# Kernel tuning notes

Hardware: AMD Instinct MI355X
Metric: run time of the kernel (lower is better)

## Reference

```python
import jax, jax.numpy as jnp
import numpy as np

TAU = 1.0
ATOL = 1e-06
MAX_ITER = 64  # bisection halves the bracket each iter; 64 iters reaches fp32 precision
N_WORKERS = 64
D = 2097152  # 2**21 coordinates


def setup_inputs() -> dict:
    key = jax.random.key(0)
    y = jax.random.normal(key, (N_WORKERS, D), dtype=jnp.float32)
    return {"y": y}


def reference(y) -> jnp.ndarray:
    # Coordinate-wise smooth (erf-based) median via bisection.
    # torch code transposes y and reduces over the last dim; equivalently we
    # reduce over the worker axis (axis 0) and keep per-coordinate state [d].
    xl = jnp.min(y, axis=0)  # [d] lower bracket
    xg = jnp.max(y, axis=0)  # [d] upper bracket

    def body(_, carry):
        xl, xg = carry
        xm = 0.5 * (xl + xg)                                  # [d]
        fm = jnp.sum(jax.lax.erf((y - xm) / TAU), axis=0)     # [d]
        left = fm > 0
        xl = jnp.where(left, xm, xl)
        xg = jnp.where(left, xg, xm)
        return xl, xg

    # Fixed trip count (no host-sync early exit). After MAX_ITER=64 halvings the
    # bracket width is far below the torch atol=1e-6 break threshold, so the
    # result matches the torch early-exit version to well within atol.
    xl, xg = jax.lax.fori_loop(0, MAX_ITER, body, (xl, xg))
    return 0.5 * (xl + xg)  # [d]
```

## Files before the change

### kernel.cpp

```cpp
#include <hip/hip_runtime.h>

typedef float v2f __attribute__((ext_vector_type(2)));

#define NW 64
#define NP 32
#define MAX_EVALS 8
#define FREEZE_TOL 7e-3f

__global__ __launch_bounds__(256, 4) void damed_median_kernel(
    const float* __restrict__ y, float* __restrict__ out, int D) {
  int d = blockIdx.x * blockDim.x + threadIdx.x;
  if (d >= D) return;

  v2f v[NP];
  v2f vmin = {3.4e38f, 3.4e38f}, vmax = {-3.4e38f, -3.4e38f}, sum2 = {0.f, 0.f};
#pragma unroll
  for (int p = 0; p < NP; ++p) {
    v2f t;
    t.x = y[(size_t)(2 * p) * (size_t)D + (size_t)d];
    t.y = y[(size_t)(2 * p + 1) * (size_t)D + (size_t)d];
    v[p] = t;
    vmin = __builtin_elementwise_min(vmin, t);
    vmax = __builtin_elementwise_max(vmax, t);
    sum2 += t;
  }
  float xl = fminf(vmin.x, vmin.y);
  float xg = fmaxf(vmax.x, vmax.y);
  float x = (sum2.x + sum2.y) * (1.0f / NW);
  x = fminf(fmaxf(x, xl), xg);

  const float B1 = 0.278393f, B2 = 0.230389f, B3 = 0.000972f, B4 = 0.078108f;
  const v2f one2 = {1.f, 1.f};
  const v2f Q1 = {B1, B1}, Q2 = {B2, B2}, Q3 = {B3, B3}, Q4 = {B4, B4};
  const v2f P1 = {B1, B1}, P2 = {2 * B2, 2 * B2};
  const v2f P3 = {3 * B3, 3 * B3}, P4 = {4 * B4, 4 * B4};

  auto evalF = [&](float xc) -> float {
    v2f fmA = {0.f, 0.f}, fmB = {0.f, 0.f};
    v2f nx = {-xc, -xc};
#pragma unroll
    for (int p = 0; p < NP; p += 2) {
      v2f tA = v[p] + nx;
      v2f tB = v[p + 1] + nx;
      v2f aA = __builtin_elementwise_max(tA, -tA);
      v2f aB = __builtin_elementwise_max(tB, -tB);
      v2f qA = __builtin_elementwise_fma(aA, Q4, Q3);
      v2f qB = __builtin_elementwise_fma(aB, Q4, Q3);
      qA = __builtin_elementwise_fma(aA, qA, Q2);
      qB = __builtin_elementwise_fma(aB, qB, Q2);
      qA = __builtin_elementwise_fma(aA, qA, Q1);
      qB = __builtin_elementwise_fma(aB, qB, Q1);
      qA = __builtin_elementwise_fma(aA, qA, one2);
      qB = __builtin_elementwise_fma(aB, qB, one2);
      v2f m = qA * qB;
      v2f r;
      r.x = __builtin_amdgcn_rcpf(m.x); r.y = __builtin_amdgcn_rcpf(m.y);
      v2f rA = r * qB;
      v2f rB = r * qA;
      rA = rA * rA; rB = rB * rB;
      rA = rA * rA; rB = rB * rB;
      v2f eA = one2 - rA;
      v2f eB = one2 - rB;
      eA.x = __builtin_copysignf(eA.x, tA.x); eA.y = __builtin_copysignf(eA.y, tA.y);
      eB.x = __builtin_copysignf(eB.x, tB.x); eB.y = __builtin_copysignf(eB.y, tB.y);
      fmA += eA; fmB += eB;
    }
    v2f s = fmA + fmB;
    return s.x + s.y;
  };

  float fm0, fd0;
  {
    v2f fmA = {0.f, 0.f}, fmB = {0.f, 0.f}, fdA = {0.f, 0.f}, fdB = {0.f, 0.f};
    v2f nx = {-x, -x};
#pragma unroll
    for (int p = 0; p < NP; p += 2) {
      v2f tA = v[p] + nx;
      v2f tB = v[p + 1] + nx;
      v2f aA = __builtin_elementwise_max(tA, -tA);
      v2f aB = __builtin_elementwise_max(tB, -tB);
      v2f qA = __builtin_elementwise_fma(aA, Q4, Q3);
      v2f qB = __builtin_elementwise_fma(aB, Q4, Q3);
      qA = __builtin_elementwise_fma(aA, qA, Q2);
      qB = __builtin_elementwise_fma(aB, qB, Q2);
      qA = __builtin_elementwise_fma(aA, qA, Q1);
      qB = __builtin_elementwise_fma(aB, qB, Q1);
      qA = __builtin_elementwise_fma(aA, qA, one2);
      qB = __builtin_elementwise_fma(aB, qB, one2);
      v2f dA = __builtin_elementwise_fma(aA, P4, P3);
      v2f dB = __builtin_elementwise_fma(aB, P4, P3);
      dA = __builtin_elementwise_fma(aA, dA, P2);
      dB = __builtin_elementwise_fma(aB, dB, P2);
      dA = __builtin_elementwise_fma(aA, dA, P1);
      dB = __builtin_elementwise_fma(aB, dB, P1);
      v2f m = qA * qB;
      v2f r;
      r.x = __builtin_amdgcn_rcpf(m.x); r.y = __builtin_amdgcn_rcpf(m.y);
      v2f rA = r * qB;
      v2f rB = r * qA;
      v2f r2A = rA * rA, r2B = rB * rB;
      v2f r4A = r2A * r2A, r4B = r2B * r2B;
      v2f r5A = r4A * rA, r5B = r4B * rB;
      fdA = __builtin_elementwise_fma(r5A, dA, fdA);
      fdB = __builtin_elementwise_fma(r5B, dB, fdB);
      v2f eA = one2 - r4A;
      v2f eB = one2 - r4B;
      eA.x = __builtin_copysignf(eA.x, tA.x); eA.y = __builtin_copysignf(eA.y, tA.y);
      eB.x = __builtin_copysignf(eB.x, tB.x); eB.y = __builtin_copysignf(eB.y, tB.y);
      fmA += eA; fmB += eB;
    }
    v2f fm2 = fmA + fmB, fd2 = fdA + fdB;
    fm0 = fm2.x + fm2.y;
    fd0 = 4.0f * (fd2.x + fd2.y);
  }
  if (fm0 > 0.f) xl = x; else xg = x;
  float xn = x + fm0 * __builtin_amdgcn_rcpf(fd0);
  bool ok = (xn >= xl) && (xn <= xg);
  float cand = ok ? xn : 0.5f * (xl + xg);
  bool frozen = (__builtin_fabsf(cand - x) <= FREEZE_TOL);
  float xprev = x, fmprev = fm0;
  x = cand;

#pragma unroll 1
  for (int e = 1; e < MAX_EVALS; ++e) {
    if (__all(frozen)) break;
    float fmc = evalF(x);
    if (fmc > 0.f) xl = x; else xg = x;
    float xs = x + fmc * (x - xprev) / (fmprev - fmc);
    bool ok2 = (xs >= xl) && (xs <= xg);
    float cand2 = ok2 ? xs : 0.5f * (xl + xg);
    float st = __builtin_fabsf(cand2 - x);
    bool done = (st <= FREEZE_TOL) || (fmc == 0.f);
    float xnew = frozen ? x : cand2;
    xprev = frozen ? xprev : x;
    fmprev = frozen ? fmprev : fmc;
    frozen = frozen || done;
    x = xnew;
  }
  out[d] = x;
}

extern "C" void kernel_launch(void* const* d_in, const int* in_sizes, int n_in,
                              void* d_out, int out_size, void* d_ws, size_t ws_size,
                              hipStream_t stream) {
  const float* y = (const float*)d_in[0];
  float* out = (float*)d_out;
  const int D = out_size;
  const int threads = 256;
  const int blocks = (D + threads - 1) / threads;
  damed_median_kernel<<<blocks, threads, 0, stream>>>(y, out, D);
}
```

Before: 118.7 us.

## Double-buffer column loads across a persistent multi-coordinate loop

Each thread now processes several coordinates (CPT=8) spaced by a grid stride, keeping two register buffers of the 64 worker values. While one coordinate's root-finding runs, the next coordinate's loads are issued, so memory latency overlaps with compute. Launch bounds drop to 2 waves per SIMD to make room for the doubled register footprint, which lowers occupancy and may cause spills.

```diff
diff --git a/kernel.cpp b/kernel.cpp
--- a/kernel.cpp
+++ b/kernel.cpp
@@ -6,28 +6,11 @@
 #define NP 32
 #define MAX_EVALS 8
 #define FREEZE_TOL 7e-3f
+#define CPT 8
 
-__global__ __launch_bounds__(256, 4) void damed_median_kernel(
-    const float* __restrict__ y, float* __restrict__ out, int D) {
+__global__ __launch_bounds__(256, 2) void damed_median_kernel(
+    const float* __restrict__ y, float* __restrict__ out, int D, int T) {
   int d = blockIdx.x * blockDim.x + threadIdx.x;
-  if (d >= D) return;
-
-  v2f v[NP];
-  v2f vmin = {3.4e38f, 3.4e38f}, vmax = {-3.4e38f, -3.4e38f}, sum2 = {0.f, 0.f};
-#pragma unroll
-  for (int p = 0; p < NP; ++p) {
-    v2f t;
-    t.x = y[(size_t)(2 * p) * (size_t)D + (size_t)d];
-    t.y = y[(size_t)(2 * p + 1) * (size_t)D + (size_t)d];
-    v[p] = t;
-    vmin = __builtin_elementwise_min(vmin, t);
-    vmax = __builtin_elementwise_max(vmax, t);
-    sum2 += t;
-  }
-  float xl = fminf(vmin.x, vmin.y);
-  float xg = fmaxf(vmax.x, vmax.y);
-  float x = (sum2.x + sum2.y) * (1.0f / NW);
-  x = fminf(fmaxf(x, xl), xg);
 
   const float B1 = 0.278393f, B2 = 0.230389f, B3 = 0.000972f, B4 = 0.078108f;
   const v2f one2 = {1.f, 1.f};
@@ -35,7 +18,34 @@
   const v2f P1 = {B1, B1}, P2 = {2 * B2, 2 * B2};
   const v2f P3 = {3 * B3, 3 * B3}, P4 = {4 * B4, 4 * B4};
 
-  auto evalF = [&](float xc) -> float {
+  v2f vA[NP], vB[NP];
+
+  auto load = [&](v2f (&v)[NP], int dc) {
+    int dcl = dc < D ? dc : D - 1;
+#pragma unroll
+    for (int p = 0; p < NP; ++p) {
+      v2f t;
+      t.x = y[(size_t)(2 * p) * (size_t)D + (size_t)dcl];
+      t.y = y[(size_t)(2 * p + 1) * (size_t)D + (size_t)dcl];
+      v[p] = t;
+    }
+  };
+
+  auto prep = [&](const v2f (&v)[NP], float& xl, float& xg, float& x) {
+    v2f vmin = {3.4e38f, 3.4e38f}, vmax = {-3.4e38f, -3.4e38f}, s = {0.f, 0.f};
+#pragma unroll
+    for (int p = 0; p < NP; ++p) {
+      vmin = __builtin_elementwise_min(vmin, v[p]);
+      vmax = __builtin_elementwise_max(vmax, v[p]);
+      s += v[p];
+    }
+    xl = fminf(vmin.x, vmin.y);
+    xg = fmaxf(vmax.x, vmax.y);
+    x = (s.x + s.y) * (1.0f / NW);
+    x = fminf(fmaxf(x, xl), xg);
+  };
+
+  auto evalF = [&](const v2f (&v)[NP], float xc) -> float {
     v2f fmA = {0.f, 0.f}, fmB = {0.f, 0.f};
     v2f nx = {-xc, -xc};
 #pragma unroll
@@ -69,75 +79,91 @@
     return s.x + s.y;
   };
 
-  float fm0, fd0;
-  {
-    v2f fmA = {0.f, 0.f}, fmB = {0.f, 0.f}, fdA = {0.f, 0.f}, fdB = {0.f, 0.f};
-    v2f nx = {-x, -x};
+  auto solve_rest = [&](const v2f (&v)[NP], float xl, float xg, float x, int dc) {
+    float fm0, fd0;
+    {
+      v2f fmA = {0.f, 0.f}, fmB = {0.f, 0.f}, fdA = {0.f, 0.f}, fdB = {0.f, 0.f};
+      v2f nx = {-x, -x};
 #pragma unroll
-    for (int p = 0; p < NP; p += 2) {
-      v2f tA = v[p] + nx;
-      v2f tB = v[p + 1] + nx;
-      v2f aA = __builtin_elementwise_max(tA, -tA);
-      v2f aB = __builtin_elementwise_max(tB, -tB);
-      v2f qA = __builtin_elementwise_fma(aA, Q4, Q3);
-      v2f qB = __builtin_elementwise_fma(aB, Q4, Q3);
-      qA = __builtin_elementwise_fma(aA, qA, Q2);
-      qB = __builtin_elementwise_fma(aB, qB, Q2);
-      qA = __builtin_elementwise_fma(aA, qA, Q1);
-      qB = __builtin_elementwise_fma(aB, qB, Q1);
-      qA = __builtin_elementwise_fma(aA, qA, one2);
-      qB = __builtin_elementwise_fma(aB, qB, one2);
-      v2f dA = __builtin_elementwise_fma(aA, P4, P3);
-      v2f dB = __builtin_elementwise_fma(aB, P4, P3);
-      dA = __builtin_elementwise_fma(aA, dA, P2);
-      dB = __builtin_elementwise_fma(aB, dB, P2);
-      dA = __builtin_elementwise_fma(aA, dA, P1);
-      dB = __builtin_elementwise_fma(aB, dB, P1);
-      v2f m = qA * qB;
-      v2f r;
-      r.x = __builtin_amdgcn_rcpf(m.x); r.y = __builtin_amdgcn_rcpf(m.y);
-      v2f rA = r * qB;
-      v2f rB = r * qA;
-      v2f r2A = rA * rA, r2B = rB * rB;
-      v2f r4A = r2A * r2A, r4B = r2B * r2B;
-      v2f r5A = r4A * rA, r5B = r4B * rB;
-      fdA = __builtin_elementwise_fma(r5A, dA, fdA);
-      fdB = __builtin_elementwise_fma(r5B, dB, fdB);
-      v2f eA = one2 - r4A;
-      v2f eB = one2 - r4B;
-      eA.x = __builtin_copysignf(eA.x, tA.x); eA.y = __builtin_copysignf(eA.y, tA.y);
-      eB.x = __builtin_copysignf(eB.x, tB.x); eB.y = __builtin_copysignf(eB.y, tB.y);
-      fmA += eA; fmB += eB;
+      for (int p = 0; p < NP; p += 2) {
+        v2f tA = v[p] + nx;
+        v2f tB = v[p + 1] + nx;
+        v2f aA = __builtin_elementwise_max(tA, -tA);
+        v2f aB = __builtin_elementwise_max(tB, -tB);
+        v2f qA = __builtin_elementwise_fma(aA, Q4, Q3);
+        v2f qB = __builtin_elementwise_fma(aB, Q4, Q3);
+        qA = __builtin_elementwise_fma(aA, qA, Q2);
+        qB = __builtin_elementwise_fma(aB, qB, Q2);
+        qA = __builtin_elementwise_fma(aA, qA, Q1);
+        qB = __builtin_elementwise_fma(aB, qB, Q1);
+        qA = __builtin_elementwise_fma(aA, qA, one2);
+        qB = __builtin_elementwise_fma(aB, qB, one2);
+        v2f dA = __builtin_elementwise_fma(aA, P4, P3);
+        v2f dB = __builtin_elementwise_fma(aB, P4, P3);
+        dA = __builtin_elementwise_fma(aA, dA, P2);
+        dB = __builtin_elementwise_fma(aB, dB, P2);
+        dA = __builtin_elementwise_fma(aA, dA, P1);
+        dB = __builtin_elementwise_fma(aB, dB, P1);
+        v2f m = qA * qB;
+        v2f r;
+        r.x = __builtin_amdgcn_rcpf(m.x); r.y = __builtin_amdgcn_rcpf(m.y);
+        v2f rA = r * qB;
+        v2f rB = r * qA;
+        v2f r2A = rA * rA, r2B = rB * rB;
+        v2f r4A = r2A * r2A, r4B = r2B * r2B;
+        v2f r5A = r4A * rA, r5B = r4B * rB;
+        fdA = __builtin_elementwise_fma(r5A, dA, fdA);
+        fdB = __builtin_elementwise_fma(r5B, dB, fdB);
+        v2f eA = one2 - r4A;
+        v2f eB = one2 - r4B;
+        eA.x = __builtin_copysignf(eA.x, tA.x); eA.y = __builtin_copysignf(eA.y, tA.y);
+        eB.x = __builtin_copysignf(eB.x, tB.x); eB.y = __builtin_copysignf(eB.y, tB.y);
+        fmA += eA; fmB += eB;
+      }
+      v2f fm2 = fmA + fmB, fd2 = fdA + fdB;
+      fm0 = fm2.x + fm2.y;
+      fd0 = 4.0f * (fd2.x + fd2.y);
     }
-    v2f fm2 = fmA + fmB, fd2 = fdA + fdB;
-    fm0 = fm2.x + fm2.y;
-    fd0 = 4.0f * (fd2.x + fd2.y);
-  }
-  if (fm0 > 0.f) xl = x; else xg = x;
-  float xn = x + fm0 * __builtin_amdgcn_rcpf(fd0);
-  bool ok = (xn >= xl) && (xn <= xg);
-  float cand = ok ? xn : 0.5f * (xl + xg);
-  bool frozen = (__builtin_fabsf(cand - x) <= FREEZE_TOL);
-  float xprev = x, fmprev = fm0;
-  x = cand;
+    if (fm0 > 0.f) xl = x; else xg = x;
+    float xn = x + fm0 * __builtin_amdgcn_rcpf(fd0);
+    bool ok = (xn >= xl) && (xn <= xg);
+    float cand = ok ? xn : 0.5f * (xl + xg);
+    bool frozen = (__builtin_fabsf(cand - x) <= FREEZE_TOL);
+    float xprev = x, fmprev = fm0;
+    x = cand;
 
 #pragma unroll 1
-  for (int e = 1; e < MAX_EVALS; ++e) {
-    if (__all(frozen)) break;
-    float fmc = evalF(x);
-    if (fmc > 0.f) xl = x; else xg = x;
-    float xs = x + fmc * (x - xprev) / (fmprev - fmc);
-    bool ok2 = (xs >= xl) && (xs <= xg);
-    float cand2 = ok2 ? xs : 0.5f * (xl + xg);
-    float st = __builtin_fabsf(cand2 - x);
-    bool done = (st <= FREEZE_TOL) || (fmc == 0.f);
-    float xnew = frozen ? x : cand2;
-    xprev = frozen ? xprev : x;
-    fmprev = frozen ? fmprev : fmc;
-    frozen = frozen || done;
-    x = xnew;
+    for (int e = 1; e < MAX_EVALS; ++e) {
+      if (__all(frozen)) break;
+      float fmc = evalF(v, x);
+      if (fmc > 0.f) xl = x; else xg = x;
+      float xs = x + fmc * (x - xprev) / (fmprev - fmc);
+      bool ok2 = (xs >= xl) && (xs <= xg);
+      float cand2 = ok2 ? xs : 0.5f * (xl + xg);
+      float st = __builtin_fabsf(cand2 - x);
+      bool done = (st <= FREEZE_TOL) || (fmc == 0.f);
+      float xnew = frozen ? x : cand2;
+      xprev = frozen ? xprev : x;
+      fmprev = frozen ? fmprev : fmc;
+      frozen = frozen || done;
+      x = xnew;
+    }
+    if (dc < D) out[dc] = x;
+  };
+
+  load(vA, d);
+#pragma unroll 1
+  for (int c = 0; c < CPT; c += 2) {
+    float xl, xg, x;
+    prep(vA, xl, xg, x);
+    load(vB, d + T);
+    solve_rest(vA, xl, xg, x, d);
+    d += T;
+    prep(vB, xl, xg, x);
+    if (c + 2 < CPT) load(vA, d + T);
+    solve_rest(vB, xl, xg, x, d);
+    d += T;
   }
-  out[d] = x;
 }
 
 extern "C" void kernel_launch(void* const* d_in, const int* in_sizes, int n_in,
@@ -147,6 +173,7 @@
   float* out = (float*)d_out;
   const int D = out_size;
   const int threads = 256;
-  const int blocks = (D + threads - 1) / threads;
-  damed_median_kernel<<<blocks, threads, 0, stream>>>(y, out, D);
+  const int blocks = (D + threads * CPT - 1) / (threads * CPT);
+  const int T = blocks * threads;
+  damed_median_kernel<<<blocks, threads, 0, stream>>>(y, out, D, T);
 }
```

Measured after the change: 129.7 us. 9.4% more time.
